# Performance work log

Measured on AMD Instinct MI355X. Metric: run time of the kernel, lower is better.

The kernel has to match this reference:

```python
import jax, jax.numpy as jnp
import numpy as np

B, L, T = 64, 128, 48
E, HE, H = 512, 1024, 1024


def setup_inputs() -> dict:
    key = jax.random.key(0)
    ks = jax.random.split(key, 20)
    s = 0.02
    inp = {
        'enc_hiddens': jax.random.normal(ks[0], (B, L, HE), jnp.float32),
        'enc_masks': jax.random.randint(ks[1], (B, L), 0, 2, jnp.int32),
        'h1_init': jax.random.normal(ks[2], (B, H), jnp.float32),
        'c1_init': jax.random.normal(ks[3], (B, H), jnp.float32),
        'h2_init': jax.random.normal(ks[4], (B, H), jnp.float32),
        'c2_init': jax.random.normal(ks[5], (B, H), jnp.float32),
        'captions': jax.random.normal(ks[6], (T, B, E), jnp.float32),
        # LSTMCell 1: input E -> hidden H
        'W_ih1': jax.random.normal(ks[7], (4 * H, E), jnp.float32) * s,
        'W_hh1': jax.random.normal(ks[8], (4 * H, H), jnp.float32) * s,
        'b_ih1': jnp.zeros((4 * H,), jnp.float32),
        'b_hh1': jnp.zeros((4 * H,), jnp.float32),
        # LSTMCell 2: input 2H -> hidden H
        'W_ih2': jax.random.normal(ks[9], (4 * H, 2 * H), jnp.float32) * s,
        'W_hh2': jax.random.normal(ks[10], (4 * H, H), jnp.float32) * s,
        'b_ih2': jnp.zeros((4 * H,), jnp.float32),
        'b_hh2': jnp.zeros((4 * H,), jnp.float32),
        # att_projection: He -> H
        'W_att': jax.random.normal(ks[11], (H, HE), jnp.float32) * s,
        'b_att': jnp.zeros((H,), jnp.float32),
        # combined_output_projection: He+H -> H
        'W_comb': jax.random.normal(ks[12], (H, HE + H), jnp.float32) * s,
        'b_comb': jnp.zeros((H,), jnp.float32),
    }
    return inp


def _lstm_cell(x, h, c, W_ih, W_hh, b_ih, b_hh):
    gates = x @ W_ih.T + b_ih + h @ W_hh.T + b_hh  # (B, 4H)
    i, f, g, o = jnp.split(gates, 4, axis=-1)
    i = jax.nn.sigmoid(i)
    f = jax.nn.sigmoid(f)
    g = jnp.tanh(g)
    o = jax.nn.sigmoid(o)
    c_new = f * c + i * g
    h_new = o * jnp.tanh(c_new)
    return h_new, c_new


def reference(enc_hiddens, enc_masks, h1_init, c1_init, h2_init, c2_init, captions,
              W_ih1, W_hh1, b_ih1, b_hh1, W_ih2, W_hh2, b_ih2, b_hh2,
              W_att, b_att, W_comb, b_comb):
    # Precompute attention projection of encoder hiddens: (B, L, H)
    enc_proj = jnp.einsum('blf,hf->blh', enc_hiddens, W_att) + b_att
    mask = enc_masks.astype(bool)  # True -> masked with -inf
    o0 = jnp.zeros((enc_hiddens.shape[0], W_hh1.shape[1]), enc_hiddens.dtype)

    def step(carry, elem):
        h1, c1, h2, c2, o_prev = carry
        h1, c1 = _lstm_cell(elem, h1, c1, W_ih1, W_hh1, b_ih1, b_hh1)
        bar = jnp.concatenate([h1, o_prev], axis=1)  # (B, 2H)
        h2, c2 = _lstm_cell(bar, h2, c2, W_ih2, W_hh2, b_ih2, b_hh2)
        e_t = jnp.einsum('bh,blh->bl', h2, enc_proj)
        e_t = jnp.where(mask, -jnp.inf, e_t)
        alpha = jax.nn.softmax(e_t, axis=1)
        a_t = jnp.einsum('bl,blf->bf', alpha, enc_hiddens)  # (B, He)
        U_t = jnp.concatenate([a_t, h2], axis=1)
        o_t = jnp.tanh(U_t @ W_comb.T + b_comb)  # dropout is identity in eval
        return (h1, c1, h2, c2, o_t), o_t

    _, outs = jax.lax.scan(step, (h1_init, c1_init, h2_init, c2_init, o0), captions)
    return outs  # (T, B, H)
```

## Files before the change

kernel.cpp:

```cpp
#include <hip/hip_runtime.h>

static constexpr int Bn = 64, Ln = 128, Tn = 48, En = 512, HEn = 1024, Hn = 1024, Gn = 4096;

typedef _Float16 h16;
typedef __attribute__((ext_vector_type(8))) _Float16 h16x8;
typedef __attribute__((ext_vector_type(2))) _Float16 h16x2;
typedef __attribute__((ext_vector_type(4))) float f32x4;

__device__ __forceinline__ float sigf(float x){ return 1.f / (1.f + expf(-x)); }

__global__ void cvt2(const float* __restrict__ in, h16x2* __restrict__ out, int n2){
  int i = blockIdx.x * blockDim.x + threadIdx.x;
  int stride = gridDim.x * blockDim.x;
  for (; i < n2; i += stride){
    float2 v = reinterpret_cast<const float2*>(in)[i];
    h16x2 o; o.x = (h16)v.x; o.y = (h16)v.y;
    out[i] = o;
  }
}

__global__ void init_state(const float* __restrict__ h1i, const float* __restrict__ c1i,
                           const float* __restrict__ h2i, const float* __restrict__ c2i,
                           h16* __restrict__ h1a, float* __restrict__ c1,
                           h16* __restrict__ h2a, float* __restrict__ c2,
                           float* __restrict__ h2f, h16* __restrict__ oh){
  int i = blockIdx.x * blockDim.x + threadIdx.x;
  if (i < Bn * Hn){
    h1a[i] = (h16)h1i[i]; c1[i] = c1i[i];
    h2a[i] = (h16)h2i[i]; c2[i] = c2i[i];
    h2f[i] = h2i[i];
    oh[i] = (h16)0.f;
  }
}

__global__ __launch_bounds__(256, 2) void gemm_lds(
    const h16* __restrict__ A, int lda,
    const h16* __restrict__ Bw, int ldb,
    const float* __restrict__ bias0, const float* __restrict__ bias1,
    float* __restrict__ outF, h16* __restrict__ outH, int ldc, int K)
{
  __shared__ __align__(16) h16 sA[2][4096];
  __shared__ __align__(16) h16 sB[2][4096];
  int tid = threadIdx.x;
  int w = tid >> 6, lane = tid & 63;
  int la = lane & 15, q = lane >> 4;
  int wr = w >> 1, wc = w & 1;
  int m0 = blockIdx.x * 128, n0 = blockIdx.y * 128;

  int srow = tid >> 2, sq = tid & 3;
  const h16* gAa = A + (size_t)(m0 + srow) * lda + sq * 8;
  const h16* gAb = gAa + (size_t)64 * lda;
  const h16* gBa = Bw + (size_t)(n0 + srow) * ldb + sq * 8;
  const h16* gBb = gBa + (size_t)64 * ldb;
  int dO = sq * 1024 + srow * 8;

  f32x4 acc[4][4];
  #pragma unroll
  for (int i = 0; i < 4; i++)
    #pragma unroll
    for (int j = 0; j < 4; j++) acc[i][j] = (f32x4){0.f, 0.f, 0.f, 0.f};

  h16x8 rAa, rAb, rBa, rBb;
  auto GLOAD = [&](int kt){
    int k0 = kt * 32;
    rAa = *reinterpret_cast<const h16x8*>(gAa + k0);
    rAb = *reinterpret_cast<const h16x8*>(gAb + k0);
    rBa = *reinterpret_cast<const h16x8*>(gBa + k0);
    rBb = *reinterpret_cast<const h16x8*>(gBb + k0);
  };
  auto SWRITE = [&](int buf){
    *reinterpret_cast<h16x8*>(&sA[buf][dO])       = rAa;
    *reinterpret_cast<h16x8*>(&sA[buf][dO + 512]) = rAb;
    *reinterpret_cast<h16x8*>(&sB[buf][dO])       = rBa;
    *reinterpret_cast<h16x8*>(&sB[buf][dO + 512]) = rBb;
  };

  int NT = K / 32;
  GLOAD(0); SWRITE(0);
  GLOAD(1);
  __syncthreads();
  for (int t = 0; t < NT; t++){
    int buf = t & 1;
    h16x8 af[4], bf[4];
    #pragma unroll
    for (int mi = 0; mi < 4; mi++)
      af[mi] = *reinterpret_cast<const h16x8*>(&sA[buf][q * 1024 + (wr * 64 + mi * 16 + la) * 8]);
    #pragma unroll
    for (int ni = 0; ni < 4; ni++)
      bf[ni] = *reinterpret_cast<const h16x8*>(&sB[buf][q * 1024 + (wc * 64 + ni * 16 + la) * 8]);
    #pragma unroll
    for (int mi = 0; mi < 4; mi++)
      #pragma unroll
      for (int ni = 0; ni < 4; ni++)
        acc[mi][ni] = __builtin_amdgcn_mfma_f32_16x16x32_f16(af[mi], bf[ni], acc[mi][ni], 0, 0, 0);
    if (t + 1 < NT){
      __syncthreads();
      SWRITE((t + 1) & 1);
      if (t + 2 < NT) GLOAD(t + 2);
      __syncthreads();
    }
  }

  #pragma unroll
  for (int mi = 0; mi < 4; mi++){
    int mrow = m0 + wr * 64 + mi * 16 + q * 4;
    #pragma unroll
    for (int ni = 0; ni < 4; ni++){
      int n = n0 + wc * 64 + ni * 16 + la;
      float bs = (bias0 ? bias0[n] : 0.f) + (bias1 ? bias1[n] : 0.f);
      #pragma unroll
      for (int r = 0; r < 4; r++){
        float v = acc[mi][ni][r] + bs;
        size_t off = (size_t)(mrow + r) * ldc + n;
        if (outF) outF[off] = v;
        else      outH[off] = (h16)v;
      }
    }
  }
}

struct PBuf { h16x8 a0, a1, a2, a3, b; };

__device__ __forceinline__ void pld(PBuf& p, const h16* __restrict__ Ap,
                                    const h16* __restrict__ Bp, int k){
  p.a0 = *reinterpret_cast<const h16x8*>(Ap + k);
  p.a1 = *reinterpret_cast<const h16x8*>(Ap + 16 * Hn + k);
  p.a2 = *reinterpret_cast<const h16x8*>(Ap + 32 * Hn + k);
  p.a3 = *reinterpret_cast<const h16x8*>(Ap + 48 * Hn + k);
  p.b  = *reinterpret_cast<const h16x8*>(Bp + k);
}
__device__ __forceinline__ void pmm(const PBuf& p, f32x4* acc){
  acc[0] = __builtin_amdgcn_mfma_f32_16x16x32_f16(p.a0, p.b, acc[0], 0, 0, 0);
  acc[1] = __builtin_amdgcn_mfma_f32_16x16x32_f16(p.a1, p.b, acc[1], 0, 0, 0);
  acc[2] = __builtin_amdgcn_mfma_f32_16x16x32_f16(p.a2, p.b, acc[2], 0, 0, 0);
  acc[3] = __builtin_amdgcn_mfma_f32_16x16x32_f16(p.a3, p.b, acc[3], 0, 0, 0);
}

template<int NS>
__device__ __forceinline__ void gseg_pf(const h16* __restrict__ Ap,
                                        const h16* __restrict__ Bp, f32x4* acc){
  PBuf p0, p1, p2, p3;
  pld(p0, Ap, Bp, 0);
  pld(p1, Ap, Bp, 32);
  pld(p2, Ap, Bp, 64);
  pld(p3, Ap, Bp, 96);
  #pragma unroll 1
  for (int s = 0; s + 4 < NS; s += 4){
    pmm(p0, acc); pld(p0, Ap, Bp, (s + 4) * 32);
    pmm(p1, acc); pld(p1, Ap, Bp, (s + 5) * 32);
    pmm(p2, acc); pld(p2, Ap, Bp, (s + 6) * 32);
    pmm(p3, acc); pld(p3, Ap, Bp, (s + 7) * 32);
  }
  pmm(p0, acc); pmm(p1, acc); pmm(p2, acc); pmm(p3, acc);
}

struct PBuf2 { h16x8 a0, a1, b; };

__device__ __forceinline__ void pld2(PBuf2& p, const h16* __restrict__ Ap,
                                     const h16* __restrict__ Bp, int k){
  p.a0 = *reinterpret_cast<const h16x8*>(Ap + k);
  p.a1 = *reinterpret_cast<const h16x8*>(Ap + 16 * Hn + k);
  p.b  = *reinterpret_cast<const h16x8*>(Bp + k);
}
__device__ __forceinline__ void pmm2(const PBuf2& p, f32x4* acc){
  acc[0] = __builtin_amdgcn_mfma_f32_16x16x32_f16(p.a0, p.b, acc[0], 0, 0, 0);
  acc[1] = __builtin_amdgcn_mfma_f32_16x16x32_f16(p.a1, p.b, acc[1], 0, 0, 0);
}

template<int NS>
__device__ __forceinline__ void gseg2_pf(const h16* __restrict__ Ap,
                                         const h16* __restrict__ Bp, f32x4* acc){
  PBuf2 p0, p1, p2, p3;
  pld2(p0, Ap, Bp, 0);
  pld2(p1, Ap, Bp, 32);
  pld2(p2, Ap, Bp, 64);
  pld2(p3, Ap, Bp, 96);
  #pragma unroll 1
  for (int s = 0; s + 4 < NS; s += 4){
    pmm2(p0, acc); pld2(p0, Ap, Bp, (s + 4) * 32);
    pmm2(p1, acc); pld2(p1, Ap, Bp, (s + 5) * 32);
    pmm2(p2, acc); pld2(p2, Ap, Bp, (s + 6) * 32);
    pmm2(p3, acc); pld2(p3, Ap, Bp, (s + 7) * 32);
  }
  pmm2(p0, acc); pmm2(p1, acc); pmm2(p2, acc); pmm2(p3, acc);
}

__global__ __launch_bounds__(512, 1) void kA(
    const h16* __restrict__ h1cur, const h16* __restrict__ h2prev, const h16* __restrict__ oh,
    h16* __restrict__ h1next, h16* __restrict__ h2cur, float* __restrict__ h2f,
    float* __restrict__ c1, float* __restrict__ c2,
    const h16* __restrict__ wih2, const h16* __restrict__ whh2, const h16* __restrict__ whh1,
    const float* __restrict__ bih2, const float* __restrict__ bhh2,
    const float* __restrict__ pre1_t, int mode)
{
  __shared__ float sg[4][2][32][17];
  int bid = blockIdx.x, tid = threadIdx.x;
  int wv = tid >> 6, lane = tid & 63;
  int g = wv & 3, kh = wv >> 2;
  int la = lane & 15, q = lane >> 4;
  bool is2 = (mode == 1) && (bid < 128);
  int unit = is2 ? bid : (mode == 1 ? bid - 128 : bid);
  int jb = unit >> 1, mh = unit & 1;
  int j0 = jb * 16;
  int r0 = mh * 32;
  bool active = is2 || (pre1_t != nullptr);

  if (active){
    f32x4 acc[2];
    acc[0] = (f32x4){0.f, 0.f, 0.f, 0.f};
    acc[1] = (f32x4){0.f, 0.f, 0.f, 0.f};
    int n0 = g * 1024 + j0;
    size_t aoff = (size_t)(r0 + la) * Hn + q * 8;
    if (is2){
      if (kh == 0){
        gseg2_pf<32>(h1cur + aoff, wih2 + (size_t)(n0 + la) * 2048 + q * 8,        acc);
        gseg2_pf<16>(oh    + aoff, wih2 + (size_t)(n0 + la) * 2048 + 1024 + q * 8, acc);
      } else {
        gseg2_pf<16>(oh     + aoff + 512, wih2 + (size_t)(n0 + la) * 2048 + 1536 + q * 8, acc);
        gseg2_pf<32>(h2prev + aoff,       whh2 + (size_t)(n0 + la) * 1024 + q * 8,        acc);
      }
    } else {
      if (kh == 0)
        gseg2_pf<16>(h1cur + aoff,       whh1 + (size_t)(n0 + la) * 1024 + q * 8,       acc);
      else
        gseg2_pf<16>(h1cur + aoff + 512, whh1 + (size_t)(n0 + la) * 1024 + 512 + q * 8, acc);
    }
    #pragma unroll
    for (int mi = 0; mi < 2; mi++)
      #pragma unroll
      for (int r = 0; r < 4; r++)
        sg[g][kh][mi * 16 + q * 4 + r][la] = acc[mi][r];
  }
  __syncthreads();
  if (active && tid < 512){
    int e = tid;
    int rl = e >> 4, col = e & 15, j = j0 + col;
    int row = r0 + rl;
    float gi = sg[0][0][rl][col] + sg[0][1][rl][col];
    float gf = sg[1][0][rl][col] + sg[1][1][rl][col];
    float gg = sg[2][0][rl][col] + sg[2][1][rl][col];
    float go = sg[3][0][rl][col] + sg[3][1][rl][col];
    if (is2){
      gi += bih2[j] + bhh2[j];
      gf += bih2[j + 1024] + bhh2[j + 1024];
      gg += bih2[j + 2048] + bhh2[j + 2048];
      go += bih2[j + 3072] + bhh2[j + 3072];
      float c_ = sigf(gf) * c2[row * Hn + j] + sigf(gi) * tanhf(gg);
      c2[row * Hn + j] = c_;
      float h_ = sigf(go) * tanhf(c_);
      h2cur[row * Hn + j] = (h16)h_;
      h2f[row * Hn + j] = h_;
    } else {
      const float* p = pre1_t + (size_t)row * Gn;
      gi += p[j]; gf += p[j + 1024]; gg += p[j + 2048]; go += p[j + 3072];
      float c_ = sigf(gf) * c1[row * Hn + j] + sigf(gi) * tanhf(gg);
      c1[row * Hn + j] = c_;
      h1next[row * Hn + j] = (h16)(sigf(go) * tanhf(c_));
    }
  }
}

__global__ __launch_bounds__(256, 2) void kB(
    const float* __restrict__ h2f, const h16* __restrict__ eph, const int* __restrict__ msk,
    float* __restrict__ ebuf,
    const h16* __restrict__ h2cur, const h16* __restrict__ wcomb, const float* __restrict__ bcomb,
    float* __restrict__ hwb)
{
  int bid = blockIdx.x, tid = threadIdx.x;
  int w = tid >> 6, lane = tid & 63;
  if (bid >= 16){
    int wv = (bid - 16) * 4 + w;
    int b = wv >> 7;
    int l = wv & 127;
    const f32x4* h2r = reinterpret_cast<const f32x4*>(h2f + (size_t)b * Hn + lane * 16);
    f32x4 hv0 = h2r[0], hv1 = h2r[1], hv2 = h2r[2], hv3 = h2r[3];
    const h16x8* er = reinterpret_cast<const h16x8*>(eph + ((size_t)b * Ln + l) * Hn + lane * 16);
    h16x8 e0 = er[0], e1 = er[1];
    float acc = 0.f;
    #pragma unroll
    for (int i = 0; i < 4; i++) acc += hv0[i] * (float)e0[i];
    #pragma unroll
    for (int i = 0; i < 4; i++) acc += hv1[i] * (float)e0[4 + i];
    #pragma unroll
    for (int i = 0; i < 4; i++) acc += hv2[i] * (float)e1[i];
    #pragma unroll
    for (int i = 0; i < 4; i++) acc += hv3[i] * (float)e1[4 + i];
    for (int off = 32; off; off >>= 1) acc += __shfl_xor(acc, off);
    if (lane == 0) ebuf[b * Ln + l] = msk[b * Ln + l] ? -1e30f : acc;
  } else {
    int hb = bid;
    int la = lane & 15, q = lane >> 4;
    int n0 = hb * 64 + w * 16;
    f32x4 acc[4];
    #pragma unroll
    for (int mi = 0; mi < 4; mi++) acc[mi] = (f32x4){0.f, 0.f, 0.f, 0.f};
    gseg_pf<32>(h2cur + la * Hn + q * 8,
                wcomb + (size_t)(n0 + la) * (HEn + Hn) + HEn + q * 8, acc);
    float bs = bcomb[n0 + la];
    #pragma unroll
    for (int mi = 0; mi < 4; mi++)
      #pragma unroll
      for (int r = 0; r < 4; r++)
        hwb[(size_t)(mi * 16 + q * 4 + r) * Hn + n0 + la] = acc[mi][r] + bs;
  }
}

__global__ __launch_bounds__(256, 2) void kC(
    int t, const float* __restrict__ ebuf,
    const h16* __restrict__ ecbh, const float* __restrict__ hwb,
    float* __restrict__ out, h16* __restrict__ oh)
{
  __shared__ float sb[Ln];
  __shared__ float rmax[4], rsum[4];
  __shared__ float sp[128][2];
  int bid = blockIdx.x;
  int b = bid >> 2;
  int jq = (bid & 3) * 256;
  int tid = threadIdx.x;
  int wv = tid >> 6;
  float e = ebuf[b * Ln + (tid & 127)];
  float m = e;
  #pragma unroll
  for (int off = 32; off; off >>= 1) m = fmaxf(m, __shfl_xor(m, off));
  if ((tid & 63) == 0) rmax[wv] = m;
  __syncthreads();
  m = fmaxf(fmaxf(rmax[0], rmax[1]), fmaxf(rmax[2], rmax[3]));
  float ex = expf(e - m);
  if (tid < 128) sb[tid] = ex;
  float s = ex;
  #pragma unroll
  for (int off = 32; off; off >>= 1) s += __shfl_xor(s, off);
  if ((tid & 63) == 0) rsum[wv] = s;
  __syncthreads();
  float rinv = 1.f / (rsum[0] + rsum[1]);

  int col = tid & 127, lh = tid >> 7;
  int j0 = jq + col * 2;
  const h16* base = ecbh + (size_t)b * Ln * Hn + j0;
  float a0 = 0.f, a1 = 0.f, c0 = 0.f, c1 = 0.f;
  int lb = lh * 64;
  #pragma unroll 8
  for (int i = 0; i < 64; i += 2){
    int l = lb + i;
    float al0 = sb[l], al1 = sb[l + 1];
    h16x2 p0 = *reinterpret_cast<const h16x2*>(base + (size_t)l * Hn);
    h16x2 p1 = *reinterpret_cast<const h16x2*>(base + (size_t)(l + 1) * Hn);
    a0 += al0 * (float)p0.x; a1 += al0 * (float)p0.y;
    c0 += al1 * (float)p1.x; c1 += al1 * (float)p1.y;
  }
  float t0 = a0 + c0, t1 = a1 + c1;
  if (lh == 1){ sp[col][0] = t0; sp[col][1] = t1; }
  __syncthreads();
  if (lh == 0){
    float g0 = (t0 + sp[col][0]) * rinv;
    float g1 = (t1 + sp[col][1]) * rinv;
    float2 hw2 = *reinterpret_cast<const float2*>(hwb + b * Hn + j0);
    float o0 = tanhf(g0 + hw2.x);
    float o1 = tanhf(g1 + hw2.y);
    *reinterpret_cast<float2*>(out + ((size_t)t * Bn + b) * Hn + j0) = make_float2(o0, o1);
    h16x2 opk; opk.x = (h16)o0; opk.y = (h16)o1;
    *reinterpret_cast<h16x2*>(oh + (size_t)b * Hn + j0) = opk;
  }
}

extern "C" void kernel_launch(void* const* d_in, const int* in_sizes, int n_in,
                              void* d_out, int out_size, void* d_ws, size_t ws_size,
                              hipStream_t stream)
{
  const float* enc   = (const float*)d_in[0];
  const int*   msk   = (const int*)  d_in[1];
  const float* h1i   = (const float*)d_in[2];
  const float* c1i   = (const float*)d_in[3];
  const float* h2i   = (const float*)d_in[4];
  const float* c2i   = (const float*)d_in[5];
  const float* caps  = (const float*)d_in[6];
  const float* Wih1  = (const float*)d_in[7];
  const float* Whh1  = (const float*)d_in[8];
  const float* bih1  = (const float*)d_in[9];
  const float* bhh1  = (const float*)d_in[10];
  const float* Wih2  = (const float*)d_in[11];
  const float* Whh2  = (const float*)d_in[12];
  const float* bih2  = (const float*)d_in[13];
  const float* bhh2  = (const float*)d_in[14];
  const float* Watt  = (const float*)d_in[15];
  const float* batt  = (const float*)d_in[16];
  const float* Wcomb = (const float*)d_in[17];
  const float* bcomb = (const float*)d_in[18];
  float* out = (float*)d_out;

  char* p = (char*)d_ws;
  auto take = [&](size_t bytes){ char* r = p; p += (bytes + 255) & ~(size_t)255; return r; };
  float* pre1   = (float*)take((size_t)Tn * Bn * Gn * 4);
  h16*   ench   = (h16*)take((size_t)Bn * Ln * HEn * 2);
  h16*   eph    = (h16*)take((size_t)Bn * Ln * Hn * 2);
  h16*   ecbh   = (h16*)take((size_t)Bn * Ln * Hn * 2);
  h16*   caph   = (h16*)take((size_t)Tn * Bn * En * 2);
  h16*   wih1h  = (h16*)take((size_t)Gn * En * 2);
  h16*   whh1h  = (h16*)take((size_t)Gn * Hn * 2);
  h16*   wih2h  = (h16*)take((size_t)Gn * 2 * Hn * 2);
  h16*   whh2h  = (h16*)take((size_t)Gn * Hn * 2);
  h16*   watth  = (h16*)take((size_t)Hn * HEn * 2);
  h16*   wcombh = (h16*)take((size_t)Hn * (HEn + Hn) * 2);
  h16*   h1b0   = (h16*)take((size_t)Bn * Hn * 2);
  h16*   h1b1   = (h16*)take((size_t)Bn * Hn * 2);
  h16*   h2b0   = (h16*)take((size_t)Bn * Hn * 2);
  h16*   h2b1   = (h16*)take((size_t)Bn * Hn * 2);
  h16*   oh     = (h16*)take((size_t)Bn * Hn * 2);
  float* c1     = (float*)take((size_t)Bn * Hn * 4);
  float* c2     = (float*)take((size_t)Bn * Hn * 4);
  float* h2f    = (float*)take((size_t)Bn * Hn * 4);
  float* ebuf   = (float*)take((size_t)Bn * Ln * 4);
  float* hwb    = (float*)take((size_t)Bn * Hn * 4);
  (void)ws_size; (void)n_in; (void)in_sizes; (void)out_size;

  auto cvt = [&](const float* src, void* dst, int n){
    int n2 = n / 2;
    int blocks = (n2 + 255) / 256; if (blocks > 2048) blocks = 2048;
    cvt2<<<blocks, 256, 0, stream>>>(src, (h16x2*)dst, n2);
  };
  cvt(enc,   ench,   Bn * Ln * HEn);
  cvt(caps,  caph,   Tn * Bn * En);
  cvt(Wih1,  wih1h,  Gn * En);
  cvt(Whh1,  whh1h,  Gn * Hn);
  cvt(Wih2,  wih2h,  Gn * 2 * Hn);
  cvt(Whh2,  whh2h,  Gn * Hn);
  cvt(Watt,  watth,  Hn * HEn);
  cvt(Wcomb, wcombh, Hn * (HEn + Hn));

  init_state<<<(Bn * Hn) / 256, 256, 0, stream>>>(h1i, c1i, h2i, c2i,
                                                  h1b0, c1, h2b0, c2, h2f, oh);

  gemm_lds<<<dim3((Tn * Bn) / 128, Gn / 128), 256, 0, stream>>>(
      caph, En, wih1h, En, bih1, bhh1, pre1, nullptr, Gn, En);
  gemm_lds<<<dim3((Bn * Ln) / 128, Hn / 128), 256, 0, stream>>>(
      ench, HEn, watth, HEn, batt, nullptr, nullptr, eph, Hn, HEn);
  gemm_lds<<<dim3((Bn * Ln) / 128, Hn / 128), 256, 0, stream>>>(
      ench, HEn, wcombh, HEn + Hn, nullptr, nullptr, nullptr, ecbh, Hn, HEn);

  kA<<<128, 512, 0, stream>>>(h1b0, h2b0, oh, h1b1, h2b1, h2f, c1, c2,
                              wih2h, whh2h, whh1h, bih2, bhh2, pre1, 0);

  h16* h1buf[2] = { h1b0, h1b1 };
  h16* h2buf[2] = { h2b0, h2b1 };
  for (int t = 0; t < Tn; t++){
    h16* h1cur  = h1buf[(t + 1) & 1];
    h16* h1next = h1buf[t & 1];
    h16* h2prev = h2buf[t & 1];
    h16* h2cur  = h2buf[(t + 1) & 1];
    const float* pre1_t = (t + 1 < Tn) ? (pre1 + (size_t)(t + 1) * Bn * Gn) : nullptr;
    kA<<<256, 512, 0, stream>>>(h1cur, h2prev, oh, h1next, h2cur, h2f, c1, c2,
                                wih2h, whh2h, whh1h, bih2, bhh2, pre1_t, 1);
    kB<<<2064, 256, 0, stream>>>(h2f, eph, msk, ebuf, h2cur, wcombh, bcomb, hwb);
    kC<<<256, 256, 0, stream>>>(t, ebuf, ecbh, hwb, out, oh);
  }
}
```

Measured before the change: 3.203 ms.

## Fuse attention-score and output-projection kernels into one per-step kernel

The separate kB (energies plus the h2·W_comb MFMA GEMM) and kC (softmax, context, tanh) launches are merged into a single kBC kernel per timestep. Each block now computes the 128 attention energies for its batch row itself, then the softmax. It computes the h2 part of the combined projection with per-thread scalar fp16 dot products against h2 staged in LDS, and reads the precomputed encoder-times-W_comb term from a transposed layout so each output column's 128 values are contiguous. This removes one launch and the ebuf/hwb round trips through global memory per step. In exchange, the energy computation is repeated by the four blocks that share a batch row, and the MFMA GEMM is replaced by uncoalesced per-thread row reads of W_comb.

New measurement: 4.048 ms. 26.4% more time.

```diff
diff --git a/kernel.cpp b/kernel.cpp
--- a/kernel.cpp
+++ b/kernel.cpp
@@ -8,6 +8,13 @@
 typedef __attribute__((ext_vector_type(4))) float f32x4;
 
 __device__ __forceinline__ float sigf(float x){ return 1.f / (1.f + expf(-x)); }
+
+__device__ __forceinline__ float dot8f(h16x8 a, h16x8 b){
+  float s = 0.f;
+  #pragma unroll
+  for (int i = 0; i < 8; i++) s += (float)a[i] * (float)b[i];
+  return s;
+}
 
 __global__ void cvt2(const float* __restrict__ in, h16x2* __restrict__ out, int n2){
   int i = blockIdx.x * blockDim.x + threadIdx.x;
@@ -117,41 +124,6 @@
       }
     }
   }
-}
-
-struct PBuf { h16x8 a0, a1, a2, a3, b; };
-
-__device__ __forceinline__ void pld(PBuf& p, const h16* __restrict__ Ap,
-                                    const h16* __restrict__ Bp, int k){
-  p.a0 = *reinterpret_cast<const h16x8*>(Ap + k);
-  p.a1 = *reinterpret_cast<const h16x8*>(Ap + 16 * Hn + k);
-  p.a2 = *reinterpret_cast<const h16x8*>(Ap + 32 * Hn + k);
-  p.a3 = *reinterpret_cast<const h16x8*>(Ap + 48 * Hn + k);
-  p.b  = *reinterpret_cast<const h16x8*>(Bp + k);
-}
-__device__ __forceinline__ void pmm(const PBuf& p, f32x4* acc){
-  acc[0] = __builtin_amdgcn_mfma_f32_16x16x32_f16(p.a0, p.b, acc[0], 0, 0, 0);
-  acc[1] = __builtin_amdgcn_mfma_f32_16x16x32_f16(p.a1, p.b, acc[1], 0, 0, 0);
-  acc[2] = __builtin_amdgcn_mfma_f32_16x16x32_f16(p.a2, p.b, acc[2], 0, 0, 0);
-  acc[3] = __builtin_amdgcn_mfma_f32_16x16x32_f16(p.a3, p.b, acc[3], 0, 0, 0);
-}
-
-template<int NS>
-__device__ __forceinline__ void gseg_pf(const h16* __restrict__ Ap,
-                                        const h16* __restrict__ Bp, f32x4* acc){
-  PBuf p0, p1, p2, p3;
-  pld(p0, Ap, Bp, 0);
-  pld(p1, Ap, Bp, 32);
-  pld(p2, Ap, Bp, 64);
-  pld(p3, Ap, Bp, 96);
-  #pragma unroll 1
-  for (int s = 0; s + 4 < NS; s += 4){
-    pmm(p0, acc); pld(p0, Ap, Bp, (s + 4) * 32);
-    pmm(p1, acc); pld(p1, Ap, Bp, (s + 5) * 32);
-    pmm(p2, acc); pld(p2, Ap, Bp, (s + 6) * 32);
-    pmm(p3, acc); pld(p3, Ap, Bp, (s + 7) * 32);
-  }
-  pmm(p0, acc); pmm(p1, acc); pmm(p2, acc); pmm(p3, acc);
 }
 
 struct PBuf2 { h16x8 a0, a1, b; };
@@ -260,69 +232,53 @@
   }
 }
 
-__global__ __launch_bounds__(256, 2) void kB(
-    const float* __restrict__ h2f, const h16* __restrict__ eph, const int* __restrict__ msk,
-    float* __restrict__ ebuf,
-    const h16* __restrict__ h2cur, const h16* __restrict__ wcomb, const float* __restrict__ bcomb,
-    float* __restrict__ hwb)
+__global__ __launch_bounds__(256, 4) void kBC(
+    int t, const float* __restrict__ h2f, const h16* __restrict__ eph,
+    const int* __restrict__ msk, const h16* __restrict__ h2cur,
+    const h16* __restrict__ wcomb, const float* __restrict__ bcomb,
+    const h16* __restrict__ ecbt, float* __restrict__ out, h16* __restrict__ oh)
 {
-  int bid = blockIdx.x, tid = threadIdx.x;
-  int w = tid >> 6, lane = tid & 63;
-  if (bid >= 16){
-    int wv = (bid - 16) * 4 + w;
-    int b = wv >> 7;
-    int l = wv & 127;
-    const f32x4* h2r = reinterpret_cast<const f32x4*>(h2f + (size_t)b * Hn + lane * 16);
-    f32x4 hv0 = h2r[0], hv1 = h2r[1], hv2 = h2r[2], hv3 = h2r[3];
-    const h16x8* er = reinterpret_cast<const h16x8*>(eph + ((size_t)b * Ln + l) * Hn + lane * 16);
-    h16x8 e0 = er[0], e1 = er[1];
-    float acc = 0.f;
-    #pragma unroll
-    for (int i = 0; i < 4; i++) acc += hv0[i] * (float)e0[i];
-    #pragma unroll
-    for (int i = 0; i < 4; i++) acc += hv1[i] * (float)e0[4 + i];
-    #pragma unroll
-    for (int i = 0; i < 4; i++) acc += hv2[i] * (float)e1[i];
-    #pragma unroll
-    for (int i = 0; i < 4; i++) acc += hv3[i] * (float)e1[4 + i];
-    for (int off = 32; off; off >>= 1) acc += __shfl_xor(acc, off);
-    if (lane == 0) ebuf[b * Ln + l] = msk[b * Ln + l] ? -1e30f : acc;
-  } else {
-    int hb = bid;
-    int la = lane & 15, q = lane >> 4;
-    int n0 = hb * 64 + w * 16;
-    f32x4 acc[4];
-    #pragma unroll
-    for (int mi = 0; mi < 4; mi++) acc[mi] = (f32x4){0.f, 0.f, 0.f, 0.f};
-    gseg_pf<32>(h2cur + la * Hn + q * 8,
-                wcomb + (size_t)(n0 + la) * (HEn + Hn) + HEn + q * 8, acc);
-    float bs = bcomb[n0 + la];
-    #pragma unroll
-    for (int mi = 0; mi < 4; mi++)
-      #pragma unroll
-      for (int r = 0; r < 4; r++)
-        hwb[(size_t)(mi * 16 + q * 4 + r) * Hn + n0 + la] = acc[mi][r] + bs;
-  }
-}
-
-__global__ __launch_bounds__(256, 2) void kC(
-    int t, const float* __restrict__ ebuf,
-    const h16* __restrict__ ecbh, const float* __restrict__ hwb,
-    float* __restrict__ out, h16* __restrict__ oh)
-{
+  __shared__ float se[Ln];
   __shared__ float sb[Ln];
   __shared__ float rmax[4], rsum[4];
-  __shared__ float sp[128][2];
+  __shared__ __align__(16) h16 sh2[Hn];
   int bid = blockIdx.x;
-  int b = bid >> 2;
-  int jq = (bid & 3) * 256;
+  int b = bid >> 2, jq = (bid & 3) * 256;
   int tid = threadIdx.x;
-  int wv = tid >> 6;
-  float e = ebuf[b * Ln + (tid & 127)];
+  int w = tid >> 6, lane = tid & 63;
+
+  reinterpret_cast<unsigned long long*>(sh2)[tid] =
+      reinterpret_cast<const unsigned long long*>(h2cur + (size_t)b * Hn)[tid];
+
+  const f32x4* h2r = reinterpret_cast<const f32x4*>(h2f + (size_t)b * Hn + lane * 16);
+  f32x4 hv0 = h2r[0], hv1 = h2r[1], hv2 = h2r[2], hv3 = h2r[3];
+  for (int gse = 0; gse < 8; gse++){
+    int l0 = w * 32 + gse * 4;
+    #pragma unroll
+    for (int li = 0; li < 4; li++){
+      int l = l0 + li;
+      const h16x8* er = reinterpret_cast<const h16x8*>(eph + ((size_t)b * Ln + l) * Hn + lane * 16);
+      h16x8 e0 = er[0], e1 = er[1];
+      float acc = 0.f;
+      #pragma unroll
+      for (int i = 0; i < 4; i++) acc += hv0[i] * (float)e0[i];
+      #pragma unroll
+      for (int i = 0; i < 4; i++) acc += hv1[i] * (float)e0[4 + i];
+      #pragma unroll
+      for (int i = 0; i < 4; i++) acc += hv2[i] * (float)e1[i];
+      #pragma unroll
+      for (int i = 0; i < 4; i++) acc += hv3[i] * (float)e1[4 + i];
+      for (int off = 32; off; off >>= 1) acc += __shfl_xor(acc, off);
+      if (lane == 0) se[l] = msk[b * Ln + l] ? -1e30f : acc;
+    }
+  }
+  __syncthreads();
+
+  float e = se[tid & 127];
   float m = e;
   #pragma unroll
   for (int off = 32; off; off >>= 1) m = fmaxf(m, __shfl_xor(m, off));
-  if ((tid & 63) == 0) rmax[wv] = m;
+  if ((tid & 63) == 0) rmax[w] = m;
   __syncthreads();
   m = fmaxf(fmaxf(rmax[0], rmax[1]), fmaxf(rmax[2], rmax[3]));
   float ex = expf(e - m);
@@ -330,37 +286,43 @@
   float s = ex;
   #pragma unroll
   for (int off = 32; off; off >>= 1) s += __shfl_xor(s, off);
-  if ((tid & 63) == 0) rsum[wv] = s;
+  if ((tid & 63) == 0) rsum[w] = s;
   __syncthreads();
   float rinv = 1.f / (rsum[0] + rsum[1]);
 
-  int col = tid & 127, lh = tid >> 7;
-  int j0 = jq + col * 2;
-  const h16* base = ecbh + (size_t)b * Ln * Hn + j0;
-  float a0 = 0.f, a1 = 0.f, c0 = 0.f, c1 = 0.f;
-  int lb = lh * 64;
-  #pragma unroll 8
-  for (int i = 0; i < 64; i += 2){
-    int l = lb + i;
-    float al0 = sb[l], al1 = sb[l + 1];
-    h16x2 p0 = *reinterpret_cast<const h16x2*>(base + (size_t)l * Hn);
-    h16x2 p1 = *reinterpret_cast<const h16x2*>(base + (size_t)(l + 1) * Hn);
-    a0 += al0 * (float)p0.x; a1 += al0 * (float)p0.y;
-    c0 += al1 * (float)p1.x; c1 += al1 * (float)p1.y;
-  }
-  float t0 = a0 + c0, t1 = a1 + c1;
-  if (lh == 1){ sp[col][0] = t0; sp[col][1] = t1; }
-  __syncthreads();
-  if (lh == 0){
-    float g0 = (t0 + sp[col][0]) * rinv;
-    float g1 = (t1 + sp[col][1]) * rinv;
-    float2 hw2 = *reinterpret_cast<const float2*>(hwb + b * Hn + j0);
-    float o0 = tanhf(g0 + hw2.x);
-    float o1 = tanhf(g1 + hw2.y);
-    *reinterpret_cast<float2*>(out + ((size_t)t * Bn + b) * Hn + j0) = make_float2(o0, o1);
-    h16x2 opk; opk.x = (h16)o0; opk.y = (h16)o1;
-    *reinterpret_cast<h16x2*>(oh + (size_t)b * Hn + j0) = opk;
-  }
+  int j = jq + tid;
+  const h16x8* wr_ = reinterpret_cast<const h16x8*>(wcomb + (size_t)j * (HEn + Hn) + HEn);
+  const h16x8* hh  = reinterpret_cast<const h16x8*>(sh2);
+  float hc0 = 0.f, hc1 = 0.f, hc2 = 0.f, hc3 = 0.f;
+  #pragma unroll 4
+  for (int i = 0; i < 128; i += 4){
+    hc0 += dot8f(wr_[i],     hh[i]);
+    hc1 += dot8f(wr_[i + 1], hh[i + 1]);
+    hc2 += dot8f(wr_[i + 2], hh[i + 2]);
+    hc3 += dot8f(wr_[i + 3], hh[i + 3]);
+  }
+  float hw = hc0 + hc1 + hc2 + hc3 + bcomb[j];
+
+  const h16x8* gr = reinterpret_cast<const h16x8*>(ecbt + (size_t)j * (Bn * Ln) + b * Ln);
+  float gc0 = 0.f, gc1 = 0.f, gc2 = 0.f, gc3 = 0.f;
+  #pragma unroll
+  for (int i = 0; i < 16; i += 4){
+    h16x8 v0 = gr[i], v1 = gr[i + 1], v2 = gr[i + 2], v3 = gr[i + 3];
+    float p0 = 0.f, p1 = 0.f, p2 = 0.f, p3 = 0.f;
+    #pragma unroll
+    for (int e2 = 0; e2 < 8; e2++){
+      p0 += (float)v0[e2] * sb[i * 8 + e2];
+      p1 += (float)v1[e2] * sb[i * 8 + 8 + e2];
+      p2 += (float)v2[e2] * sb[i * 8 + 16 + e2];
+      p3 += (float)v3[e2] * sb[i * 8 + 24 + e2];
+    }
+    gc0 += p0; gc1 += p1; gc2 += p2; gc3 += p3;
+  }
+  float g = (gc0 + gc1 + gc2 + gc3) * rinv;
+
+  float o = tanhf(g + hw);
+  out[((size_t)t * Bn + b) * Hn + j] = o;
+  oh[(size_t)b * Hn + j] = (h16)o;
 }
 
 extern "C" void kernel_launch(void* const* d_in, const int* in_sizes, int n_in,
@@ -393,7 +355,7 @@
   float* pre1   = (float*)take((size_t)Tn * Bn * Gn * 4);
   h16*   ench   = (h16*)take((size_t)Bn * Ln * HEn * 2);
   h16*   eph    = (h16*)take((size_t)Bn * Ln * Hn * 2);
-  h16*   ecbh   = (h16*)take((size_t)Bn * Ln * Hn * 2);
+  h16*   ecbt   = (h16*)take((size_t)Hn * Bn * Ln * 2);
   h16*   caph   = (h16*)take((size_t)Tn * Bn * En * 2);
   h16*   wih1h  = (h16*)take((size_t)Gn * En * 2);
   h16*   whh1h  = (h16*)take((size_t)Gn * Hn * 2);
@@ -409,8 +371,6 @@
   float* c1     = (float*)take((size_t)Bn * Hn * 4);
   float* c2     = (float*)take((size_t)Bn * Hn * 4);
   float* h2f    = (float*)take((size_t)Bn * Hn * 4);
-  float* ebuf   = (float*)take((size_t)Bn * Ln * 4);
-  float* hwb    = (float*)take((size_t)Bn * Hn * 4);
   (void)ws_size; (void)n_in; (void)in_sizes; (void)out_size;
 
   auto cvt = [&](const float* src, void* dst, int n){
@@ -434,8 +394,8 @@
       caph, En, wih1h, En, bih1, bhh1, pre1, nullptr, Gn, En);
   gemm_lds<<<dim3((Bn * Ln) / 128, Hn / 128), 256, 0, stream>>>(
       ench, HEn, watth, HEn, batt, nullptr, nullptr, eph, Hn, HEn);
-  gemm_lds<<<dim3((Bn * Ln) / 128, Hn / 128), 256, 0, stream>>>(
-      ench, HEn, wcombh, HEn + Hn, nullptr, nullptr, nullptr, ecbh, Hn, HEn);
+  gemm_lds<<<dim3(Hn / 128, (Bn * Ln) / 128), 256, 0, stream>>>(
+      wcombh, HEn + Hn, ench, HEn, nullptr, nullptr, nullptr, ecbt, Bn * Ln, HEn);
 
   kA<<<128, 512, 0, stream>>>(h1b0, h2b0, oh, h1b1, h2b1, h2f, c1, c2,
                               wih2h, whh2h, whh1h, bih2, bhh2, pre1, 0);
@@ -450,7 +410,6 @@
     const float* pre1_t = (t + 1 < Tn) ? (pre1 + (size_t)(t + 1) * Bn * Gn) : nullptr;
     kA<<<256, 512, 0, stream>>>(h1cur, h2prev, oh, h1next, h2cur, h2f, c1, c2,
                                 wih2h, whh2h, whh1h, bih2, bhh2, pre1_t, 1);
-    kB<<<2064, 256, 0, stream>>>(h2f, eph, msk, ebuf, h2cur, wcombh, bcomb, hwb);
-    kC<<<256, 256, 0, stream>>>(t, ebuf, ecbh, hwb, out, oh);
-  }
-}
+    kBC<<<256, 256, 0, stream>>>(t, h2f, eph, msk, h2cur, wcombh, bcomb, ecbt, out, oh);
+  }
+}
```

## Restructure LSTM gate kernel to full-batch tiles with 4-way K split; fuse conversions

Applied to the files above, without the earlier changes.

The per-step LSTM gate kernel now gives each block all 64 batch rows for a 16-column gate slice, using 1024 threads with a four-way K split and an LDS reduction. Before, the batch was split into two 32-row halves with a two-way K split. Each weight slice is therefore read once per step rather than twice, and the grid shrinks from 256 to 128 blocks. Separately, the eight fp32-to-fp16 conversion launches are merged into a single multi-job kernel to cut launch overhead. The trade-off is fewer blocks per step with larger LDS use and more reduction work, which may lower CU utilisation.

Result: slower. 4.215 ms (+31.6%).

```diff
diff --git a/kernel.cpp b/kernel.cpp
--- a/kernel.cpp
+++ b/kernel.cpp
@@ -9,13 +9,25 @@
 
 __device__ __forceinline__ float sigf(float x){ return 1.f / (1.f + expf(-x)); }
 
-__global__ void cvt2(const float* __restrict__ in, h16x2* __restrict__ out, int n2){
-  int i = blockIdx.x * blockDim.x + threadIdx.x;
+struct CvtJobs {
+  const float* src[8];
+  h16x2* dst[8];
+  int n2[8];
+};
+
+__global__ void cvt_all(CvtJobs jobs){
   int stride = gridDim.x * blockDim.x;
-  for (; i < n2; i += stride){
-    float2 v = reinterpret_cast<const float2*>(in)[i];
-    h16x2 o; o.x = (h16)v.x; o.y = (h16)v.y;
-    out[i] = o;
+  int gid = blockIdx.x * blockDim.x + threadIdx.x;
+  #pragma unroll
+  for (int s = 0; s < 8; s++){
+    const float* src = jobs.src[s];
+    h16x2* dst = jobs.dst[s];
+    int n2 = jobs.n2[s];
+    for (int i = gid; i < n2; i += stride){
+      float2 v = reinterpret_cast<const float2*>(src)[i];
+      h16x2 o; o.x = (h16)v.x; o.y = (h16)v.y;
+      dst[i] = o;
+    }
   }
 }
 
@@ -154,38 +166,7 @@
   pmm(p0, acc); pmm(p1, acc); pmm(p2, acc); pmm(p3, acc);
 }
 
-struct PBuf2 { h16x8 a0, a1, b; };
-
-__device__ __forceinline__ void pld2(PBuf2& p, const h16* __restrict__ Ap,
-                                     const h16* __restrict__ Bp, int k){
-  p.a0 = *reinterpret_cast<const h16x8*>(Ap + k);
-  p.a1 = *reinterpret_cast<const h16x8*>(Ap + 16 * Hn + k);
-  p.b  = *reinterpret_cast<const h16x8*>(Bp + k);
-}
-__device__ __forceinline__ void pmm2(const PBuf2& p, f32x4* acc){
-  acc[0] = __builtin_amdgcn_mfma_f32_16x16x32_f16(p.a0, p.b, acc[0], 0, 0, 0);
-  acc[1] = __builtin_amdgcn_mfma_f32_16x16x32_f16(p.a1, p.b, acc[1], 0, 0, 0);
-}
-
-template<int NS>
-__device__ __forceinline__ void gseg2_pf(const h16* __restrict__ Ap,
-                                         const h16* __restrict__ Bp, f32x4* acc){
-  PBuf2 p0, p1, p2, p3;
-  pld2(p0, Ap, Bp, 0);
-  pld2(p1, Ap, Bp, 32);
-  pld2(p2, Ap, Bp, 64);
-  pld2(p3, Ap, Bp, 96);
-  #pragma unroll 1
-  for (int s = 0; s + 4 < NS; s += 4){
-    pmm2(p0, acc); pld2(p0, Ap, Bp, (s + 4) * 32);
-    pmm2(p1, acc); pld2(p1, Ap, Bp, (s + 5) * 32);
-    pmm2(p2, acc); pld2(p2, Ap, Bp, (s + 6) * 32);
-    pmm2(p3, acc); pld2(p3, Ap, Bp, (s + 7) * 32);
-  }
-  pmm2(p0, acc); pmm2(p1, acc); pmm2(p2, acc); pmm2(p3, acc);
-}
-
-__global__ __launch_bounds__(512, 1) void kA(
+__global__ __launch_bounds__(1024, 1) void kA(
     const h16* __restrict__ h1cur, const h16* __restrict__ h2prev, const h16* __restrict__ oh,
     h16* __restrict__ h1next, h16* __restrict__ h2cur, float* __restrict__ h2f,
     float* __restrict__ c1, float* __restrict__ c2,
@@ -193,53 +174,44 @@
     const float* __restrict__ bih2, const float* __restrict__ bhh2,
     const float* __restrict__ pre1_t, int mode)
 {
-  __shared__ float sg[4][2][32][17];
+  __shared__ float sg[4][4][64][17];
   int bid = blockIdx.x, tid = threadIdx.x;
   int wv = tid >> 6, lane = tid & 63;
-  int g = wv & 3, kh = wv >> 2;
+  int g = wv & 3, kq = wv >> 2;
   int la = lane & 15, q = lane >> 4;
-  bool is2 = (mode == 1) && (bid < 128);
-  int unit = is2 ? bid : (mode == 1 ? bid - 128 : bid);
-  int jb = unit >> 1, mh = unit & 1;
-  int j0 = jb * 16;
-  int r0 = mh * 32;
+  bool is2 = (mode == 1) && (bid < 64);
+  int unit = is2 ? bid : (mode == 1 ? bid - 64 : bid);
+  int j0 = unit * 16;
   bool active = is2 || (pre1_t != nullptr);
 
   if (active){
-    f32x4 acc[2];
-    acc[0] = (f32x4){0.f, 0.f, 0.f, 0.f};
-    acc[1] = (f32x4){0.f, 0.f, 0.f, 0.f};
+    f32x4 acc[4];
+    #pragma unroll
+    for (int mi = 0; mi < 4; mi++) acc[mi] = (f32x4){0.f, 0.f, 0.f, 0.f};
     int n0 = g * 1024 + j0;
-    size_t aoff = (size_t)(r0 + la) * Hn + q * 8;
+    size_t aoff = (size_t)la * Hn + q * 8;
     if (is2){
-      if (kh == 0){
-        gseg2_pf<32>(h1cur + aoff, wih2 + (size_t)(n0 + la) * 2048 + q * 8,        acc);
-        gseg2_pf<16>(oh    + aoff, wih2 + (size_t)(n0 + la) * 2048 + 1024 + q * 8, acc);
-      } else {
-        gseg2_pf<16>(oh     + aoff + 512, wih2 + (size_t)(n0 + la) * 2048 + 1536 + q * 8, acc);
-        gseg2_pf<32>(h2prev + aoff,       whh2 + (size_t)(n0 + la) * 1024 + q * 8,        acc);
-      }
+      int ko = kq * 256;
+      gseg_pf<8>(h1cur  + aoff + ko, wih2 + (size_t)(n0 + la) * 2048 + ko + q * 8,        acc);
+      gseg_pf<8>(oh     + aoff + ko, wih2 + (size_t)(n0 + la) * 2048 + 1024 + ko + q * 8, acc);
+      gseg_pf<8>(h2prev + aoff + ko, whh2 + (size_t)(n0 + la) * 1024 + ko + q * 8,        acc);
     } else {
-      if (kh == 0)
-        gseg2_pf<16>(h1cur + aoff,       whh1 + (size_t)(n0 + la) * 1024 + q * 8,       acc);
-      else
-        gseg2_pf<16>(h1cur + aoff + 512, whh1 + (size_t)(n0 + la) * 1024 + 512 + q * 8, acc);
+      int ko = kq * 256;
+      gseg_pf<8>(h1cur  + aoff + ko, whh1 + (size_t)(n0 + la) * 1024 + ko + q * 8,        acc);
     }
     #pragma unroll
-    for (int mi = 0; mi < 2; mi++)
+    for (int mi = 0; mi < 4; mi++)
       #pragma unroll
       for (int r = 0; r < 4; r++)
-        sg[g][kh][mi * 16 + q * 4 + r][la] = acc[mi][r];
+        sg[g][kq][mi * 16 + q * 4 + r][la] = acc[mi][r];
   }
   __syncthreads();
-  if (active && tid < 512){
-    int e = tid;
-    int rl = e >> 4, col = e & 15, j = j0 + col;
-    int row = r0 + rl;
-    float gi = sg[0][0][rl][col] + sg[0][1][rl][col];
-    float gf = sg[1][0][rl][col] + sg[1][1][rl][col];
-    float gg = sg[2][0][rl][col] + sg[2][1][rl][col];
-    float go = sg[3][0][rl][col] + sg[3][1][rl][col];
+  if (active){
+    int row = tid >> 4, col = tid & 15, j = j0 + col;
+    float gi = sg[0][0][row][col] + sg[0][1][row][col] + sg[0][2][row][col] + sg[0][3][row][col];
+    float gf = sg[1][0][row][col] + sg[1][1][row][col] + sg[1][2][row][col] + sg[1][3][row][col];
+    float gg = sg[2][0][row][col] + sg[2][1][row][col] + sg[2][2][row][col] + sg[2][3][row][col];
+    float go = sg[3][0][row][col] + sg[3][1][row][col] + sg[3][2][row][col] + sg[3][3][row][col];
     if (is2){
       gi += bih2[j] + bhh2[j];
       gf += bih2[j + 1024] + bhh2[j + 1024];
@@ -413,19 +385,16 @@
   float* hwb    = (float*)take((size_t)Bn * Hn * 4);
   (void)ws_size; (void)n_in; (void)in_sizes; (void)out_size;
 
-  auto cvt = [&](const float* src, void* dst, int n){
-    int n2 = n / 2;
-    int blocks = (n2 + 255) / 256; if (blocks > 2048) blocks = 2048;
-    cvt2<<<blocks, 256, 0, stream>>>(src, (h16x2*)dst, n2);
-  };
-  cvt(enc,   ench,   Bn * Ln * HEn);
-  cvt(caps,  caph,   Tn * Bn * En);
-  cvt(Wih1,  wih1h,  Gn * En);
-  cvt(Whh1,  whh1h,  Gn * Hn);
-  cvt(Wih2,  wih2h,  Gn * 2 * Hn);
-  cvt(Whh2,  whh2h,  Gn * Hn);
-  cvt(Watt,  watth,  Hn * HEn);
-  cvt(Wcomb, wcombh, Hn * (HEn + Hn));
+  CvtJobs jobs;
+  jobs.src[0] = enc;   jobs.dst[0] = (h16x2*)ench;   jobs.n2[0] = Bn * Ln * HEn / 2;
+  jobs.src[1] = caps;  jobs.dst[1] = (h16x2*)caph;   jobs.n2[1] = Tn * Bn * En / 2;
+  jobs.src[2] = Wih1;  jobs.dst[2] = (h16x2*)wih1h;  jobs.n2[2] = Gn * En / 2;
+  jobs.src[3] = Whh1;  jobs.dst[3] = (h16x2*)whh1h;  jobs.n2[3] = Gn * Hn / 2;
+  jobs.src[4] = Wih2;  jobs.dst[4] = (h16x2*)wih2h;  jobs.n2[4] = Gn * 2 * Hn / 2;
+  jobs.src[5] = Whh2;  jobs.dst[5] = (h16x2*)whh2h;  jobs.n2[5] = Gn * Hn / 2;
+  jobs.src[6] = Watt;  jobs.dst[6] = (h16x2*)watth;  jobs.n2[6] = Hn * HEn / 2;
+  jobs.src[7] = Wcomb; jobs.dst[7] = (h16x2*)wcombh; jobs.n2[7] = Hn * (HEn + Hn) / 2;
+  cvt_all<<<2048, 256, 0, stream>>>(jobs);
 
   init_state<<<(Bn * Hn) / 256, 256, 0, stream>>>(h1i, c1i, h2i, c2i,
                                                   h1b0, c1, h2b0, c2, h2f, oh);
@@ -437,7 +406,7 @@
   gemm_lds<<<dim3((Bn * Ln) / 128, Hn / 128), 256, 0, stream>>>(
       ench, HEn, wcombh, HEn + Hn, nullptr, nullptr, nullptr, ecbh, Hn, HEn);
 
-  kA<<<128, 512, 0, stream>>>(h1b0, h2b0, oh, h1b1, h2b1, h2f, c1, c2,
+  kA<<<64, 1024, 0, stream>>>(h1b0, h2b0, oh, h1b1, h2b1, h2f, c1, c2,
                               wih2h, whh2h, whh1h, bih2, bhh2, pre1, 0);
 
   h16* h1buf[2] = { h1b0, h1b1 };
@@ -448,8 +417,8 @@
     h16* h2prev = h2buf[t & 1];
     h16* h2cur  = h2buf[(t + 1) & 1];
     const float* pre1_t = (t + 1 < Tn) ? (pre1 + (size_t)(t + 1) * Bn * Gn) : nullptr;
-    kA<<<256, 512, 0, stream>>>(h1cur, h2prev, oh, h1next, h2cur, h2f, c1, c2,
-                                wih2h, whh2h, whh1h, bih2, bhh2, pre1_t, 1);
+    kA<<<128, 1024, 0, stream>>>(h1cur, h2prev, oh, h1next, h2cur, h2f, c1, c2,
+                                 wih2h, whh2h, whh1h, bih2, bhh2, pre1_t, 1);
     kB<<<2064, 256, 0, stream>>>(h2f, eph, msk, ebuf, h2cur, wcombh, bcomb, hwb);
     kC<<<256, 256, 0, stream>>>(t, ebuf, ecbh, hwb, out, oh);
   }
```
